# Performance work log

Hardware: AMD Instinct MI355X
Metric: run time of the kernel (lower is better)

## Reference

```python
import jax, jax.numpy as jnp
import numpy as np

B, N = 16, 4096
NPOINT, NSAMPLE = 1024, 32
RADIUS = 0.2
D_FEAT = 64
C_IN = 3 + D_FEAT  # 67
MLP = [64, 64, 128]
EPS = 1e-5  # torch BatchNorm2d default


def setup_inputs() -> dict:
    key = jax.random.key(0)
    ks = jax.random.split(key, 10)
    inp = {
        "xyz": jax.random.uniform(ks[0], (B, 3, N), dtype=jnp.float32),
        "points": jax.random.normal(ks[1], (B, D_FEAT, N), dtype=jnp.float32),
    }
    last = C_IN
    for i, out_c in enumerate(MLP):
        kw = jax.random.fold_in(ks[2], i)
        inp[f"w{i}"] = jax.random.normal(kw, (out_c, last), dtype=jnp.float32) * (1.0 / np.sqrt(last))
        inp[f"b{i}"] = jnp.zeros((out_c,), dtype=jnp.float32)
        inp[f"g{i}"] = jnp.ones((out_c,), dtype=jnp.float32)
        inp[f"bt{i}"] = jnp.zeros((out_c,), dtype=jnp.float32)
        last = out_c
    return inp


def _fps(xyz_t, npoint):
    # xyz_t: [B, N, 3]; deterministic init at index 0 (torch version uses randint)
    b, n, _ = xyz_t.shape
    init_dist = jnp.full((b, n), 1e10, dtype=xyz_t.dtype)
    init_far = jnp.zeros((b,), dtype=jnp.int32)

    def step(carry, _):
        dist, far = carry
        centroid = jnp.take_along_axis(xyz_t, far[:, None, None], axis=1)  # [B,1,3]
        d = jnp.sum((xyz_t - centroid) ** 2, axis=-1)  # [B,N]
        dist = jnp.minimum(dist, d)
        return (dist, jnp.argmax(dist, axis=-1).astype(jnp.int32)), far

    _, cent = jax.lax.scan(step, (init_dist, init_far), None, length=npoint)
    return cent.T  # [B, npoint]


def _ball_query(xyz_t, new_xyz, radius, nsample):
    # xyz_t: [B,N,3], new_xyz: [B,S,3] -> idx [B,S,nsample]
    n = xyz_t.shape[1]
    d = (jnp.sum(new_xyz ** 2, -1)[:, :, None]
         + jnp.sum(xyz_t ** 2, -1)[:, None, :]
         - 2.0 * jnp.einsum('bsc,bnc->bsn', new_xyz, xyz_t))  # [B,S,N]
    gi = jnp.where(d > radius ** 2, n, jnp.arange(n, dtype=jnp.int32)[None, None, :])
    gi = jnp.sort(gi, axis=-1)[:, :, :nsample]
    # replace out-of-ball slots (== N) with the first valid index (centroid itself, dist 0)
    gi = jnp.where(gi == n, gi[:, :, :1], gi)
    return gi


def _gather(pts_t, idx):
    # pts_t: [B,N,C], idx: [B,S,K] -> [B,S,K,C]
    return jax.vmap(lambda p, i: p[i])(pts_t, idx)


def reference(xyz, points, w0, b0, g0, bt0, w1, b1, g1, bt1, w2, b2, g2, bt2):
    xyz_t = xyz.transpose(0, 2, 1)        # [B,N,3]
    pts_t = points.transpose(0, 2, 1)     # [B,N,D]

    cent_idx = _fps(xyz_t, NPOINT)                       # [B,S]
    new_xyz = jnp.take_along_axis(xyz_t, cent_idx[:, :, None], axis=1)  # [B,S,3]
    idx = _ball_query(xyz_t, new_xyz, RADIUS, NSAMPLE)   # [B,S,K]

    grouped_xyz = _gather(xyz_t, idx) - new_xyz[:, :, None, :]  # [B,S,K,3]
    grouped_pts = _gather(pts_t, idx)                           # [B,S,K,D]
    feat = jnp.concatenate([grouped_xyz, grouped_pts], axis=-1)  # [B,S,K,67]

    params = [(w0, b0, g0, bt0), (w1, b1, g1, bt1), (w2, b2, g2, bt2)]
    for w, b, g, bt in params:
        feat = jnp.einsum('bskc,oc->bsko', feat, w) + b  # 1x1 Conv2d
        mu = jnp.mean(feat, axis=(0, 1, 2))              # BatchNorm2d (train-mode batch stats)
        var = jnp.mean((feat - mu) ** 2, axis=(0, 1, 2))
        feat = (feat - mu) * jax.lax.rsqrt(var + EPS) * g + bt
        feat = jax.nn.relu(feat)

    new_points = jnp.max(feat, axis=2)  # max over nsample -> [B,S,C_out]
    return new_xyz.transpose(0, 2, 1), new_points.transpose(0, 2, 1)
```

## Files before the change

### kernel.cpp

```cpp
#include <hip/hip_runtime.h>
#include <cstdint>
#include <cstddef>

#define B_    16
#define N_    4096
#define S_    1024
#define K_    32
#define CNT_F 524288.0f
#define EPS_  1e-5f

#define SEG_    8
#define SEGLEN_ (N_ / SEG_)

#define OFF_NXYZ 0u
#define OFF_IDX  196608u
#define OFF_PTST 2293760u
#define OFF_PRE  20119552u
#define OFF_PRE2 87228416u
#define OFF_PART 154337280u
#define OFF_MM3  171114496u
#define OFF_ACC  187891712u

typedef _Float16 half8 __attribute__((ext_vector_type(8)));

__device__ __forceinline__ float dot4(float acc, float4 f, float4 wt) {
  return fmaf(f.w, wt.w, fmaf(f.z, wt.z, fmaf(f.y, wt.y, fmaf(f.x, wt.x, acc))));
}

template <int CTRL, int RM>
__device__ __forceinline__ uint64_t dpp_max64(uint64_t k) {
  int lo = __builtin_amdgcn_update_dpp((int)(uint32_t)k, (int)(uint32_t)k,
                                       CTRL, RM, 0xf, false);
  int hi = __builtin_amdgcn_update_dpp((int)(uint32_t)(k >> 32),
                                       (int)(uint32_t)(k >> 32),
                                       CTRL, RM, 0xf, false);
  uint64_t o = ((uint64_t)(uint32_t)hi << 32) | (uint32_t)lo;
  double m = fmax(__longlong_as_double((long long)k),
                  __longlong_as_double((long long)o));
  return (uint64_t)__double_as_longlong(m);
}

__global__ __launch_bounds__(256) void fps_tr_kernel(
    const float* __restrict__ xyz, const float* __restrict__ pts,
    float* __restrict__ nxyz, float* __restrict__ out0,
    float* __restrict__ ptsT) {
#pragma clang fp contract(off)
  __shared__ __align__(16) char smem[61504];
  int t = threadIdx.x;

  if (blockIdx.x >= B_) {
    float* tile = (float*)smem;
    int blk = blockIdx.x - B_;
    int b = blk >> 6;
    int n0 = (blk & 63) << 6;
    int wave = t >> 6, ln = t & 63;
    int n = n0 + ln;
    for (int cc = wave; cc < 68; cc += 4) {
      float v;
      if (cc < 3)       v = xyz[(size_t)(b * 3 + cc) * N_ + n];
      else if (cc < 67) v = pts[(size_t)(b * 64 + (cc - 3)) * N_ + n];
      else              v = 0.f;
      tile[ln * 69 + cc] = v;
    }
    __syncthreads();
    for (int f = t; f < 64 * 68; f += 256) {
      int r = f / 68, c = f - r * 68;
      ptsT[(size_t)(b * N_ + n0 + r) * 68 + c] = tile[r * 69 + c];
    }
    return;
  }

  float*    sx    = (float*)smem;
  float*    sy    = sx + N_;
  float*    sz    = sy + N_;
  float*    scent = sz + N_;
  uint64_t* skey  = (uint64_t*)(scent + 3 * S_);

  int b = blockIdx.x;
  const float* xb = xyz + (size_t)b * 3 * N_;
  float xr[16], yr[16], zr[16], dist[16];
  uint32_t Larr[16];
#pragma unroll
  for (int j = 0; j < 16; ++j) {
    int i = j * 256 + t;
    float x = xb[i], y = xb[N_ + i], z = xb[2 * N_ + i];
    xr[j] = x; yr[j] = y; zr[j] = z;
    sx[i] = x; sy[i] = y; sz[i] = z;
    dist[j] = 1e10f;
    Larr[j] = 0x7FFFFFFFu ^ (uint32_t)(j * 256 + t);
  }
  __syncthreads();

  int far = 0, par = 0;
  for (int s = 0; s < S_; ++s) {
    float cx = sx[far], cy = sy[far], cz = sz[far];
    if (t == 0) {
      scent[s * 3]     = cx;
      scent[s * 3 + 1] = cy;
      scent[s * 3 + 2] = cz;
    }
    uint64_t ku[16];
#pragma unroll
    for (int j = 0; j < 16; ++j) {
      float dx = xr[j] - cx, dy = yr[j] - cy, dz = zr[j] - cz;
      float d = dx * dx + dy * dy + dz * dz;
      float nd = fminf(dist[j], d);
      dist[j] = nd;
      ku[j] = ((uint64_t)__float_as_uint(nd) << 31) | Larr[j];
    }
#pragma unroll
    for (int st = 1; st < 16; st <<= 1) {
#pragma unroll
      for (int j0 = 0; j0 < 16; j0 += (st << 1)) {
        double a = __longlong_as_double((long long)ku[j0]);
        double c2 = __longlong_as_double((long long)ku[j0 + st]);
        ku[j0] = (uint64_t)__double_as_longlong(fmax(a, c2));
      }
    }
    uint64_t k = ku[0];
    k = dpp_max64<0x121, 0xf>(k);
    k = dpp_max64<0x122, 0xf>(k);
    k = dpp_max64<0x124, 0xf>(k);
    k = dpp_max64<0x128, 0xf>(k);
    k = dpp_max64<0x142, 0xa>(k);
    k = dpp_max64<0x143, 0xc>(k);
    if ((t & 63) == 63) skey[par * 4 + (t >> 6)] = k;
    __syncthreads();
    ulonglong2 p0 = *(const ulonglong2*)&skey[par * 4];
    ulonglong2 p1 = *(const ulonglong2*)&skey[par * 4 + 2];
    uint64_t m = p0.x;
    if (p0.y > m) m = p0.y;
    if (p1.x > m) m = p1.x;
    if (p1.y > m) m = p1.y;
    far = (int)((~(uint32_t)m) & 0xFFFu);
    par ^= 1;
  }
  __syncthreads();
  for (int f = t; f < 3 * S_; f += 256)
    nxyz[(size_t)b * 3 * S_ + f] = scent[f];
  for (int s = t; s < S_; s += 256) {
    out0[(size_t)b * 3 * S_ + s]          = scent[s * 3];
    out0[(size_t)b * 3 * S_ + S_ + s]     = scent[s * 3 + 1];
    out0[(size_t)b * 3 * S_ + 2 * S_ + s] = scent[s * 3 + 2];
  }
}

__global__ __launch_bounds__(64) void bq_seg_kernel(
    const float* __restrict__ xyz, const float* __restrict__ nxyz,
    int* __restrict__ segidx, int* __restrict__ segcnt) {
#pragma clang fp contract(off)
  int q = blockIdx.x * 64 + threadIdx.x;
  int seg = blockIdx.y;
  int b = q >> 10;
  const float* xb = xyz + (size_t)b * 3 * N_;
  float cx = nxyz[(size_t)q * 3];
  float cy = nxyz[(size_t)q * 3 + 1];
  float cz = nxyz[(size_t)q * 3 + 2];
  float A = fmaf(cz, cz, fmaf(cy, cy, cx * cx));
  int* out = segidx + ((size_t)q * SEG_ + seg) * K_;
  int found = 0;
  int i0 = seg * SEGLEN_;
  for (int i = i0; i < i0 + SEGLEN_; ++i) {
    float x = xb[i], y = xb[N_ + i], z = xb[2 * N_ + i];
    float Bv  = fmaf(z, z, fmaf(y, y, x * x));
    float dot = fmaf(cz, z, fmaf(cy, y, cx * x));
    float d = fmaf(-2.0f, dot, A + Bv);
    if (d <= 0.04f) {
      out[found] = i;
      ++found;
      if (found >= K_) break;
    }
  }
  segcnt[q * SEG_ + seg] = found;
}

__global__ __launch_bounds__(64) void bq_merge_kernel(
    const int* __restrict__ segidx, const int* __restrict__ segcnt,
    int* __restrict__ idxb) {
  int q = blockIdx.x * 64 + threadIdx.x;
  int* out = idxb + (size_t)q * K_;
  int found = 0, first_i = -1;
#pragma unroll
  for (int s = 0; s < SEG_; ++s) {
    int c = segcnt[q * SEG_ + s];
    const int* src = segidx + ((size_t)q * SEG_ + s) * K_;
    for (int k = 0; k < c && found < K_; ++k) {
      int v = src[k];
      if (first_i < 0) first_i = v;
      out[found++] = v;
    }
  }
  for (int sfill = found; sfill < K_; ++sfill) out[sfill] = first_i;
}

__global__ __launch_bounds__(128) void convA_kernel(
    const float* __restrict__ ptsT, const float* __restrict__ nxyz,
    const int* __restrict__ idxb, const float* __restrict__ w0,
    const float* __restrict__ b0, _Float16* __restrict__ pre,
    float* __restrict__ part) {
  __shared__ __align__(16) float sfeat[32 * 72];
  __shared__ __align__(16) float sw[64 * 76];
  __shared__ float red0[64 * 8], red1[64 * 8];
  __shared__ __align__(16) _Float16 sstage[2048];
  __shared__ int sidx[32];
  int g = blockIdx.x;
  int t = threadIdx.x;
  int b = g >> 10;
  if (t < 32) sidx[t] = idxb[(size_t)g * K_ + t];
  for (int f = t; f < 64 * 68; f += 128) {
    int c = f / 68, ci = f - c * 68;
    sw[c * 76 + ci] = (ci < 67) ? w0[c * 67 + ci] : 0.f;
  }
  const float* nx = nxyz + (size_t)g * 3;
  float ctr0 = nx[0], ctr1 = nx[1], ctr2 = nx[2];
  __syncthreads();
  for (int f = t; f < 32 * 17; f += 128) {
    int k = f / 17, q = f - k * 17;
    float4 v = *(const float4*)&ptsT[(size_t)(b * N_ + sidx[k]) * 68 + q * 4];
    if (q == 0) { v.x -= ctr0; v.y -= ctr1; v.z -= ctr2; }
    *(float4*)&sfeat[k * 72 + q * 4] = v;
  }
  __syncthreads();
  int kq = t & 7, cq = t >> 3;
  float acc[4][4] = {};
  for (int ci = 0; ci < 68; ci += 4) {
    float4 fv[4], wv[4];
#pragma unroll
    for (int kk = 0; kk < 4; ++kk) fv[kk] = *(const float4*)&sfeat[(kq + 8 * kk) * 72 + ci];
#pragma unroll
    for (int cc = 0; cc < 4; ++cc) wv[cc] = *(const float4*)&sw[(cq + 16 * cc) * 76 + ci];
#pragma unroll
    for (int kk = 0; kk < 4; ++kk)
#pragma unroll
      for (int cc = 0; cc < 4; ++cc)
        acc[kk][cc] = dot4(acc[kk][cc], fv[kk], wv[cc]);
  }
#pragma unroll
  for (int cc = 0; cc < 4; ++cc) {
    int c = cq + 16 * cc;
    float bias = b0[c];
    float s1 = 0.f, s2 = 0.f;
#pragma unroll
    for (int kk = 0; kk < 4; ++kk) {
      float v = acc[kk][cc] + bias;
      sstage[(kq + 8 * kk) * 64 + c] = (_Float16)v;
      s1 += v; s2 += v * v;
    }
    red0[c * 8 + kq] = s1; red1[c * 8 + kq] = s2;
  }
  __syncthreads();
  if (t < 64) {
    float s1 = 0.f, s2 = 0.f;
#pragma unroll
    for (int qn = 0; qn < 8; ++qn) { s1 += red0[t * 8 + qn]; s2 += red1[t * 8 + qn]; }
    part[(size_t)g * 256 + t] = s1;
    part[(size_t)g * 256 + 64 + t] = s2;
  }
  uint4* dst = (uint4*)(pre + (size_t)g * 2048);
  const uint4* srcv = (const uint4*)sstage;
  dst[t] = srcv[t];
  dst[t + 128] = srcv[t + 128];
}

__global__ __launch_bounds__(256) void red_kernel(
    const float* __restrict__ part, float* __restrict__ accum) {
  int t = threadIdx.x;
  size_t base = (size_t)blockIdx.x * 64 * 256 + t;
  float a = 0.f;
#pragma unroll 8
  for (int r = 0; r < 64; ++r) a += part[base + (size_t)r * 256];
  atomicAdd(accum + t, a);
}

__global__ __launch_bounds__(128) void convB_kernel(
    const _Float16* __restrict__ pre, const float* __restrict__ accum,
    const float* __restrict__ gam, const float* __restrict__ bet,
    const float* __restrict__ w1, const float* __restrict__ b1,
    _Float16* __restrict__ pre2, float* __restrict__ part) {
  __shared__ __align__(16) float sfeat[32 * 72];
  __shared__ __align__(16) float sw[64 * 76];
  __shared__ float red0[64 * 8], red1[64 * 8];
  __shared__ __align__(16) _Float16 sstage[2048];
  __shared__ float ssc[64], ssh[64];
  int g = blockIdx.x;
  int t = threadIdx.x;
  if (t < 64) {
    float mu = accum[t] * (1.f / CNT_F);
    float var = accum[64 + t] * (1.f / CNT_F) - mu * mu;
    float sc = gam[t] / sqrtf(var + EPS_);
    ssc[t] = sc; ssh[t] = bet[t] - mu * sc;
  }
  for (int m = t; m < 1024; m += 128) {
    int c = m >> 4, ci = (m & 15) * 4;
    *(float4*)&sw[c * 76 + ci] = *(const float4*)&w1[m * 4];
  }
  __syncthreads();
  {
    const half8* src8 = (const half8*)(pre + (size_t)g * 2048);
    int r = t >> 2, c0 = (t & 3) * 16;
    half8 h0 = src8[t * 2], h1 = src8[t * 2 + 1];
#pragma unroll
    for (int e = 0; e < 8; ++e) {
      float v = (float)h0[e] * ssc[c0 + e] + ssh[c0 + e];
      sfeat[r * 72 + c0 + e] = fmaxf(v, 0.f);
    }
#pragma unroll
    for (int e = 0; e < 8; ++e) {
      float v = (float)h1[e] * ssc[c0 + 8 + e] + ssh[c0 + 8 + e];
      sfeat[r * 72 + c0 + 8 + e] = fmaxf(v, 0.f);
    }
  }
  __syncthreads();
  int kq = t & 7, cq = t >> 3;
  float acc[4][4] = {};
  for (int ci = 0; ci < 64; ci += 4) {
    float4 fv[4], wv[4];
#pragma unroll
    for (int kk = 0; kk < 4; ++kk) fv[kk] = *(const float4*)&sfeat[(kq + 8 * kk) * 72 + ci];
#pragma unroll
    for (int cc = 0; cc < 4; ++cc) wv[cc] = *(const float4*)&sw[(cq + 16 * cc) * 76 + ci];
#pragma unroll
    for (int kk = 0; kk < 4; ++kk)
#pragma unroll
      for (int cc = 0; cc < 4; ++cc)
        acc[kk][cc] = dot4(acc[kk][cc], fv[kk], wv[cc]);
  }
#pragma unroll
  for (int cc = 0; cc < 4; ++cc) {
    int c = cq + 16 * cc;
    float bias = b1[c];
    float s1 = 0.f, s2 = 0.f;
#pragma unroll
    for (int kk = 0; kk < 4; ++kk) {
      float v = acc[kk][cc] + bias;
      sstage[(kq + 8 * kk) * 64 + c] = (_Float16)v;
      s1 += v; s2 += v * v;
    }
    red0[c * 8 + kq] = s1; red1[c * 8 + kq] = s2;
  }
  __syncthreads();
  if (t < 64) {
    float s1 = 0.f, s2 = 0.f;
#pragma unroll
    for (int qn = 0; qn < 8; ++qn) { s1 += red0[t * 8 + qn]; s2 += red1[t * 8 + qn]; }
    part[(size_t)g * 256 + t] = s1;
    part[(size_t)g * 256 + 64 + t] = s2;
  }
  uint4* dst = (uint4*)(pre2 + (size_t)g * 2048);
  const uint4* srcv = (const uint4*)sstage;
  dst[t] = srcv[t];
  dst[t + 128] = srcv[t + 128];
}

__global__ __launch_bounds__(256) void convC_kernel(
    const _Float16* __restrict__ pre2, const float* __restrict__ accum,
    const float* __restrict__ gam, const float* __restrict__ bet,
    const float* __restrict__ w2, const float* __restrict__ b2,
    float* __restrict__ mm, float* __restrict__ part) {
  __shared__ __align__(16) float sfeat[32 * 72];
  __shared__ __align__(16) float sw[128 * 76];
  __shared__ float red0[128 * 8], red1[128 * 8];
  __shared__ float rmax[128 * 8], rmin[128 * 8];
  __shared__ float ssc[64], ssh[64];
  int g = blockIdx.x;
  int t = threadIdx.x;
  if (t < 64) {
    float mu = accum[t] * (1.f / CNT_F);
    float var = accum[64 + t] * (1.f / CNT_F) - mu * mu;
    float sc = gam[t] / sqrtf(var + EPS_);
    ssc[t] = sc; ssh[t] = bet[t] - mu * sc;
  }
  for (int m = t; m < 2048; m += 256) {
    int c = m >> 4, ci = (m & 15) * 4;
    *(float4*)&sw[c * 76 + ci] = *(const float4*)&w2[m * 4];
  }
  __syncthreads();
  {
    const half8* src8 = (const half8*)(pre2 + (size_t)g * 2048);
    int r = t >> 3, c0 = (t & 7) * 8;
    half8 h0 = src8[t];
#pragma unroll
    for (int e = 0; e < 8; ++e) {
      float v = (float)h0[e] * ssc[c0 + e] + ssh[c0 + e];
      sfeat[r * 72 + c0 + e] = fmaxf(v, 0.f);
    }
  }
  __syncthreads();
  int kq = t & 7, cq = t >> 3;
  float acc[4][4] = {};
  for (int ci = 0; ci < 64; ci += 4) {
    float4 fv[4], wv[4];
#pragma unroll
    for (int kk = 0; kk < 4; ++kk) fv[kk] = *(const float4*)&sfeat[(kq + 8 * kk) * 72 + ci];
#pragma unroll
    for (int cc = 0; cc < 4; ++cc) wv[cc] = *(const float4*)&sw[(cq + 32 * cc) * 76 + ci];
#pragma unroll
    for (int kk = 0; kk < 4; ++kk)
#pragma unroll
      for (int cc = 0; cc < 4; ++cc)
        acc[kk][cc] = dot4(acc[kk][cc], fv[kk], wv[cc]);
  }
#pragma unroll
  for (int cc = 0; cc < 4; ++cc) {
    int c = cq + 32 * cc;
    float bias = b2[c];
    float s1 = 0.f, s2 = 0.f, mx = -3.4e38f, mn = 3.4e38f;
#pragma unroll
    for (int kk = 0; kk < 4; ++kk) {
      float v = acc[kk][cc] + bias;
      s1 += v; s2 += v * v;
      mx = fmaxf(mx, v); mn = fminf(mn, v);
    }
    red0[c * 8 + kq] = s1; red1[c * 8 + kq] = s2;
    rmax[c * 8 + kq] = mx; rmin[c * 8 + kq] = mn;
  }
  __syncthreads();
  if (t < 128) {
    float s1 = 0.f, s2 = 0.f, mx = -3.4e38f, mn = 3.4e38f;
#pragma unroll
    for (int qn = 0; qn < 8; ++qn) {
      s1 += red0[t * 8 + qn]; s2 += red1[t * 8 + qn];
      mx = fmaxf(mx, rmax[t * 8 + qn]); mn = fminf(mn, rmin[t * 8 + qn]);
    }
    part[(size_t)g * 256 + t] = s1;
    part[(size_t)g * 256 + 128 + t] = s2;
    mm[(size_t)g * 256 + t] = mx;
    mm[(size_t)g * 256 + 128 + t] = mn;
  }
}

__global__ __launch_bounds__(256) void fin_kernel(
    const float* __restrict__ mm, const float* __restrict__ accum,
    const float* __restrict__ gam, const float* __restrict__ bet,
    float* __restrict__ out1) {
  __shared__ float tile[128 * 65];
  __shared__ float ssc[128], ssh[128];
  int blk = blockIdx.x;
  int b = blk >> 4;
  int s0 = (blk & 15) << 6;
  int t = threadIdx.x;
  if (t < 128) {
    float mu = accum[t] * (1.f / CNT_F);
    float var = accum[128 + t] * (1.f / CNT_F) - mu * mu;
    float sc = gam[t] / sqrtf(var + EPS_);
    ssc[t] = sc; ssh[t] = bet[t] - mu * sc;
  }
  __syncthreads();
  for (int f = t; f < 64 * 128; f += 256) {
    int sl = f >> 7, c = f & 127;
    const float* row = mm + (size_t)(b * S_ + s0 + sl) * 256;
    float sc = ssc[c];
    float v = (sc >= 0.f) ? row[c] : row[128 + c];
    tile[c * 65 + sl] = fmaxf(v * sc + ssh[c], 0.f);
  }
  __syncthreads();
  for (int f = t; f < 128 * 64; f += 256) {
    int c = f >> 6, sl = f & 63;
    out1[(size_t)b * 131072 + c * 1024 + s0 + sl] = tile[c * 65 + sl];
  }
}

extern "C" void kernel_launch(void* const* d_in, const int* in_sizes, int n_in,
                              void* d_out, int out_size, void* d_ws, size_t ws_size,
                              hipStream_t stream) {
  const float* xyz = (const float*)d_in[0];
  const float* pts = (const float*)d_in[1];
  const float* w0  = (const float*)d_in[2];
  const float* b0  = (const float*)d_in[3];
  const float* g0  = (const float*)d_in[4];
  const float* bt0 = (const float*)d_in[5];
  const float* w1  = (const float*)d_in[6];
  const float* b1  = (const float*)d_in[7];
  const float* g1  = (const float*)d_in[8];
  const float* bt1 = (const float*)d_in[9];
  const float* w2  = (const float*)d_in[10];
  const float* b2  = (const float*)d_in[11];
  const float* g2  = (const float*)d_in[12];
  const float* bt2 = (const float*)d_in[13];
  float* out = (float*)d_out;

  char* ws = (char*)d_ws;
  float*    nxyz  = (float*)(ws + OFF_NXYZ);
  int*      idxb  = (int*)(ws + OFF_IDX);
  float*    ptsT  = (float*)(ws + OFF_PTST);
  _Float16* pre   = (_Float16*)(ws + OFF_PRE);
  _Float16* pre2  = (_Float16*)(ws + OFF_PRE2);
  float*    part  = (float*)(ws + OFF_PART);
  float*    mm    = (float*)(ws + OFF_MM3);
  float*    accum = (float*)(ws + OFF_ACC);
  int*      segidx = (int*)(ws + OFF_PRE);
  int*      segcnt = (int*)(ws + OFF_PRE + 16777216u);

  (void)hipMemsetAsync(accum, 0, 3 * 256 * sizeof(float), stream);

  fps_tr_kernel<<<B_ + B_ * (N_ / 64), 256, 0, stream>>>(xyz, pts, nxyz, out,
                                                         ptsT);
  bq_seg_kernel<<<dim3((B_ * S_) / 64, SEG_), 64, 0, stream>>>(xyz, nxyz,
                                                               segidx, segcnt);
  bq_merge_kernel<<<(B_ * S_) / 64, 64, 0, stream>>>(segidx, segcnt, idxb);

  convA_kernel<<<B_ * S_, 128, 0, stream>>>(ptsT, nxyz, idxb, w0, b0, pre, part);
  red_kernel<<<256, 256, 0, stream>>>(part, accum);
  convB_kernel<<<B_ * S_, 128, 0, stream>>>(pre, accum, g0, bt0, w1, b1, pre2, part);
  red_kernel<<<256, 256, 0, stream>>>(part, accum + 256);
  convC_kernel<<<B_ * S_, 256, 0, stream>>>(pre2, accum + 256, g1, bt1, w2, b2, mm, part);
  red_kernel<<<256, 256, 0, stream>>>(part, accum + 512);
  fin_kernel<<<B_ * (S_ / 64), 256, 0, stream>>>(mm, accum + 512, g2, bt2,
                                                 out + B_ * 3 * S_);
}
```

Before: 1.348 ms.

## Fuse ball-query merge into convA, prefetch FPS centroid, vectorize ball query

```diff
diff --git a/kernel.cpp b/kernel.cpp
--- a/kernel.cpp
+++ b/kernel.cpp
@@ -13,7 +13,6 @@
 #define SEGLEN_ (N_ / SEG_)
 
 #define OFF_NXYZ 0u
-#define OFF_IDX  196608u
 #define OFF_PTST 2293760u
 #define OFF_PRE  20119552u
 #define OFF_PRE2 87228416u
@@ -89,11 +88,11 @@
     dist[j] = 1e10f;
     Larr[j] = 0x7FFFFFFFu ^ (uint32_t)(j * 256 + t);
   }
-  __syncthreads();
-
-  int far = 0, par = 0;
+  float cx = xb[0], cy = xb[N_], cz = xb[2 * N_];
+  __syncthreads();
+
+  int par = 0;
   for (int s = 0; s < S_; ++s) {
-    float cx = sx[far], cy = sy[far], cz = sz[far];
     if (t == 0) {
       scent[s * 3]     = cx;
       scent[s * 3 + 1] = cy;
@@ -128,11 +127,19 @@
     __syncthreads();
     ulonglong2 p0 = *(const ulonglong2*)&skey[par * 4];
     ulonglong2 p1 = *(const ulonglong2*)&skey[par * 4 + 2];
-    uint64_t m = p0.x;
-    if (p0.y > m) m = p0.y;
-    if (p1.x > m) m = p1.x;
-    if (p1.y > m) m = p1.y;
-    far = (int)((~(uint32_t)m) & 0xFFFu);
+    uint64_t k0 = p0.x, k1 = p0.y, k2 = p1.x, k3 = p1.y;
+    int i0 = (int)((~(uint32_t)k0) & 0xFFFu);
+    int i1 = (int)((~(uint32_t)k1) & 0xFFFu);
+    int i2 = (int)((~(uint32_t)k2) & 0xFFFu);
+    int i3 = (int)((~(uint32_t)k3) & 0xFFFu);
+    float X0 = sx[i0], Y0 = sy[i0], Z0 = sz[i0];
+    float X1 = sx[i1], Y1 = sy[i1], Z1 = sz[i1];
+    float X2 = sx[i2], Y2 = sy[i2], Z2 = sz[i2];
+    float X3 = sx[i3], Y3 = sy[i3], Z3 = sz[i3];
+    uint64_t m = k0; cx = X0; cy = Y0; cz = Z0;
+    if (k1 > m) { m = k1; cx = X1; cy = Y1; cz = Z1; }
+    if (k2 > m) { m = k2; cx = X2; cy = Y2; cz = Z2; }
+    if (k3 > m) { m = k3; cx = X3; cy = Y3; cz = Z3; }
     par ^= 1;
   }
   __syncthreads();
@@ -160,59 +167,72 @@
   int* out = segidx + ((size_t)q * SEG_ + seg) * K_;
   int found = 0;
   int i0 = seg * SEGLEN_;
-  for (int i = i0; i < i0 + SEGLEN_; ++i) {
-    float x = xb[i], y = xb[N_ + i], z = xb[2 * N_ + i];
-    float Bv  = fmaf(z, z, fmaf(y, y, x * x));
-    float dot = fmaf(cz, z, fmaf(cy, y, cx * x));
-    float d = fmaf(-2.0f, dot, A + Bv);
-    if (d <= 0.04f) {
-      out[found] = i;
-      ++found;
-      if (found >= K_) break;
-    }
-  }
+#define BQ_POINT(xx, yy, zz, ii)                                   \
+  {                                                                \
+    float x = (xx), y = (yy), z = (zz);                            \
+    float Bv  = fmaf(z, z, fmaf(y, y, x * x));                     \
+    float dot = fmaf(cz, z, fmaf(cy, y, cx * x));                  \
+    float d = fmaf(-2.0f, dot, A + Bv);                            \
+    if (d <= 0.04f) {                                              \
+      out[found] = (ii);                                           \
+      ++found;                                                     \
+      if (found >= K_) goto done;                                  \
+    }                                                              \
+  }
+  for (int i = i0; i < i0 + SEGLEN_; i += 4) {
+    float4 xv = *(const float4*)&xb[i];
+    float4 yv = *(const float4*)&xb[N_ + i];
+    float4 zv = *(const float4*)&xb[2 * N_ + i];
+    BQ_POINT(xv.x, yv.x, zv.x, i)
+    BQ_POINT(xv.y, yv.y, zv.y, i + 1)
+    BQ_POINT(xv.z, yv.z, zv.z, i + 2)
+    BQ_POINT(xv.w, yv.w, zv.w, i + 3)
+  }
+done:
   segcnt[q * SEG_ + seg] = found;
-}
-
-__global__ __launch_bounds__(64) void bq_merge_kernel(
-    const int* __restrict__ segidx, const int* __restrict__ segcnt,
-    int* __restrict__ idxb) {
-  int q = blockIdx.x * 64 + threadIdx.x;
-  int* out = idxb + (size_t)q * K_;
-  int found = 0, first_i = -1;
-#pragma unroll
-  for (int s = 0; s < SEG_; ++s) {
-    int c = segcnt[q * SEG_ + s];
-    const int* src = segidx + ((size_t)q * SEG_ + s) * K_;
-    for (int k = 0; k < c && found < K_; ++k) {
-      int v = src[k];
-      if (first_i < 0) first_i = v;
-      out[found++] = v;
-    }
-  }
-  for (int sfill = found; sfill < K_; ++sfill) out[sfill] = first_i;
+#undef BQ_POINT
 }
 
 __global__ __launch_bounds__(128) void convA_kernel(
     const float* __restrict__ ptsT, const float* __restrict__ nxyz,
-    const int* __restrict__ idxb, const float* __restrict__ w0,
-    const float* __restrict__ b0, _Float16* __restrict__ pre,
-    float* __restrict__ part) {
+    const int* __restrict__ segidx, const int* __restrict__ segcnt,
+    const float* __restrict__ w0, const float* __restrict__ b0,
+    _Float16* __restrict__ pre, float* __restrict__ part) {
   __shared__ __align__(16) float sfeat[32 * 72];
   __shared__ __align__(16) float sw[64 * 76];
   __shared__ float red0[64 * 8], red1[64 * 8];
   __shared__ __align__(16) _Float16 sstage[2048];
   __shared__ int sidx[32];
+  __shared__ int scnt[8];
   int g = blockIdx.x;
   int t = threadIdx.x;
   int b = g >> 10;
-  if (t < 32) sidx[t] = idxb[(size_t)g * K_ + t];
+  if (t < 8) scnt[t] = segcnt[(size_t)g * SEG_ + t];
   for (int f = t; f < 64 * 68; f += 128) {
     int c = f / 68, ci = f - c * 68;
     sw[c * 76 + ci] = (ci < 67) ? w0[c * 67 + ci] : 0.f;
   }
   const float* nx = nxyz + (size_t)g * 3;
   float ctr0 = nx[0], ctr1 = nx[1], ctr2 = nx[2];
+  __syncthreads();
+  if (t < 32) {
+    int c0 = scnt[0], c1 = scnt[1], c2 = scnt[2], c3 = scnt[3];
+    int c4 = scnt[4], c5 = scnt[5], c6 = scnt[6], c7 = scnt[7];
+    int r = t, sel = -1, off = 0;
+#define MSTEP(cs, s)                                  \
+    if (sel < 0) {                                    \
+      if (r < (cs)) { sel = (s); off = r; }           \
+      else r -= (cs);                                 \
+    }
+    MSTEP(c0, 0) MSTEP(c1, 1) MSTEP(c2, 2) MSTEP(c3, 3)
+    MSTEP(c4, 4) MSTEP(c5, 5) MSTEP(c6, 6) MSTEP(c7, 7)
+#undef MSTEP
+    int f0 = (c0 > 0) ? 0 : (c1 > 0) ? 1 : (c2 > 0) ? 2 : (c3 > 0) ? 3
+           : (c4 > 0) ? 4 : (c5 > 0) ? 5 : (c6 > 0) ? 6 : 7;
+    int sseg = (sel >= 0) ? sel : f0;
+    int soff = (sel >= 0) ? off : 0;
+    sidx[t] = segidx[((size_t)g * SEG_ + sseg) * K_ + soff];
+  }
   __syncthreads();
   for (int f = t; f < 32 * 17; f += 128) {
     int k = f / 17, q = f - k * 17;
@@ -481,15 +501,14 @@
 
   char* ws = (char*)d_ws;
   float*    nxyz  = (float*)(ws + OFF_NXYZ);
-  int*      idxb  = (int*)(ws + OFF_IDX);
   float*    ptsT  = (float*)(ws + OFF_PTST);
   _Float16* pre   = (_Float16*)(ws + OFF_PRE);
   _Float16* pre2  = (_Float16*)(ws + OFF_PRE2);
   float*    part  = (float*)(ws + OFF_PART);
   float*    mm    = (float*)(ws + OFF_MM3);
   float*    accum = (float*)(ws + OFF_ACC);
-  int*      segidx = (int*)(ws + OFF_PRE);
-  int*      segcnt = (int*)(ws + OFF_PRE + 16777216u);
+  int*      segidx = (int*)(ws + OFF_PRE2);
+  int*      segcnt = (int*)(ws + OFF_PRE2 + 16777216u);
 
   (void)hipMemsetAsync(accum, 0, 3 * 256 * sizeof(float), stream);
 
@@ -497,9 +516,9 @@
                                                          ptsT);
   bq_seg_kernel<<<dim3((B_ * S_) / 64, SEG_), 64, 0, stream>>>(xyz, nxyz,
                                                                segidx, segcnt);
-  bq_merge_kernel<<<(B_ * S_) / 64, 64, 0, stream>>>(segidx, segcnt, idxb);
-
-  convA_kernel<<<B_ * S_, 128, 0, stream>>>(ptsT, nxyz, idxb, w0, b0, pre, part);
+
+  convA_kernel<<<B_ * S_, 128, 0, stream>>>(ptsT, nxyz, segidx, segcnt, w0, b0,
+                                            pre, part);
   red_kernel<<<256, 256, 0, stream>>>(part, accum);
   convB_kernel<<<B_ * S_, 128, 0, stream>>>(pre, accum, g0, bt0, w1, b1, pre2, part);
   red_kernel<<<256, 256, 0, stream>>>(part, accum + 256);
```

Result: no change. 1.364 ms (+1.2%).
